# Kernel optimization log

Hardware: AMD Instinct MI355X
Metric: run time of the kernel (lower is better)

The kernel has to match this reference:

```python
import jax, jax.numpy as jnp
import numpy as np

NT, C, B, N, H, E = 32768, 128, 64, 512, 4, 524288  # total nodes, channels, graphs, nodes/graph, heads, edges
DH = C // H
EPS = 1e-5


def batchnorm(x, g, b):
    # BatchNorm1d over the node dimension (training-mode batch statistics)
    m = x.mean(axis=0)
    v = x.var(axis=0)
    return (x - m) * jax.lax.rsqrt(v + EPS) * g + b


def setup_inputs() -> dict:
    key = jax.random.key(0)
    ks = jax.random.split(key, 8)
    s = 1.0 / np.sqrt(C)
    return dict(
        x=jax.random.normal(ks[0], (NT, C), jnp.float32),
        edge_index=jax.random.randint(ks[1], (2, E), 0, NT, dtype=jnp.int32),
        Wc=jax.random.normal(ks[2], (C, C), jnp.float32) * s,
        bc=jnp.zeros((C,), jnp.float32),
        in_proj_w=jax.random.normal(ks[3], (3 * C, C), jnp.float32) * s,
        in_proj_b=jnp.zeros((3 * C,), jnp.float32),
        out_proj_w=jax.random.normal(ks[4], (C, C), jnp.float32) * s,
        out_proj_b=jnp.zeros((C,), jnp.float32),
        gn1=jnp.ones((C,), jnp.float32), bn1=jnp.zeros((C,), jnp.float32),
        gn2=jnp.ones((C,), jnp.float32), bn2=jnp.zeros((C,), jnp.float32),
        gn3=jnp.ones((C,), jnp.float32), bn3=jnp.zeros((C,), jnp.float32),
        Wm1=jax.random.normal(ks[5], (2 * C, C), jnp.float32) * s,
        bm1=jnp.zeros((2 * C,), jnp.float32),
        Wm2=jax.random.normal(ks[6], (C, 2 * C), jnp.float32) / np.sqrt(2 * C),
        bm2=jnp.zeros((C,), jnp.float32),
    )


def reference(x, edge_index, Wc, bc, in_proj_w, in_proj_b, out_proj_w, out_proj_b,
              gn1, bn1, gn2, bn2, gn3, bn3, Wm1, bm1, Wm2, bm2):
    # --- local branch: mean-aggregation message passing + linear + residual + BN ---
    src, dst = edge_index[0], edge_index[1]
    agg = jax.ops.segment_sum(x[src], dst, num_segments=NT)            # [NT, C]
    cnt = jax.ops.segment_sum(jnp.ones((E, 1), x.dtype), dst, num_segments=NT)
    agg = agg / jnp.maximum(cnt, 1.0)
    h_local = agg @ Wc.T + bc + x                                       # dropout p=0 -> no-op
    h_local = batchnorm(h_local, gn1, bn1)

    # --- global branch: to_dense_batch (equal-size graphs -> reshape) + MHA ---
    hd = x.reshape(B, N, C)
    qkv = hd @ in_proj_w.T + in_proj_b                                  # [B, N, 3C]
    q, k, v = jnp.split(qkv, 3, axis=-1)
    q = q.reshape(B, N, H, DH).transpose(0, 2, 1, 3)                    # [B, H, N, DH]
    k = k.reshape(B, N, H, DH).transpose(0, 2, 1, 3)
    v = v.reshape(B, N, H, DH).transpose(0, 2, 1, 3)
    scores = jnp.einsum('bhqd,bhkd->bhqk', q, k) / np.sqrt(DH)          # [B, H, N, N]
    attn = jax.nn.softmax(scores, axis=-1)
    o = jnp.einsum('bhqk,bhkd->bhqd', attn, v)                          # [B, H, N, DH]
    o = o.transpose(0, 2, 1, 3).reshape(B, N, C)
    h_attn = (o @ out_proj_w.T + out_proj_b).reshape(NT, C) + x
    h_attn = batchnorm(h_attn, gn2, bn2)

    # --- combine + MLP + final norm ---
    out = h_local + h_attn
    out = out + (jax.nn.relu(out @ Wm1.T + bm1) @ Wm2.T + bm2)
    return batchnorm(out, gn3, bn3)
```

## Files before the change

kernel.cpp:

```cpp
#include <hip/hip_runtime.h>
#include <cstddef>

#define NT    32768
#define CCH   128
#define BB    64
#define NNODE 512
#define NHEAD 4
#define DHEAD 32
#define EE    524288
#define EPS   1e-5f
#define MAXDEG 96

typedef unsigned short u16;
typedef unsigned int   u32;
typedef __attribute__((ext_vector_type(8))) short short8;
typedef __attribute__((ext_vector_type(4))) short short4v;
typedef __attribute__((ext_vector_type(4))) float f32x4;

__device__ __forceinline__ float b2f(u32 w) { return __uint_as_float(w << 16); }
__device__ __forceinline__ u16 f2b(float f) {
    u32 u = __float_as_uint(f);
    u += 0x7FFF + ((u >> 16) & 1);
    return (u16)(u >> 16);
}

__global__ __launch_bounds__(256) void prep_kernel(const float* __restrict__ x,
                                                   const float* __restrict__ Wc,
                                                   const float* __restrict__ Wqkv,
                                                   const float* __restrict__ Wo,
                                                   const float* __restrict__ Wm1,
                                                   const float* __restrict__ Wm2,
                                                   u16* __restrict__ xb,
                                                   u16* __restrict__ Wcb,
                                                   u16* __restrict__ Wqkvb,
                                                   u16* __restrict__ Wob,
                                                   u16* __restrict__ Wm1b,
                                                   u16* __restrict__ Wm2b,
                                                   const int* __restrict__ ei,
                                                   int* __restrict__ cursor,
                                                   int* __restrict__ bucket) {
    if (blockIdx.x >= 2120) {
        int e = (blockIdx.x - 2120) * 256 + threadIdx.x;
        int src = ei[e];
        int dst = ei[EE + e];
        int pos = atomicAdd(cursor + dst, 1);
        if (pos < MAXDEG) bucket[dst * MAXDEG + pos] = src;
        return;
    }
    int r = blockIdx.x * 256 + threadIdx.x;
    const float* src; u16* dst;
    if (r < 524288) { src = x; dst = xb; }
    else if ((r -= 524288) < 2048) { src = Wc; dst = Wcb; }
    else if ((r -= 2048) < 6144) { src = Wqkv; dst = Wqkvb; }
    else if ((r -= 6144) < 2048) { src = Wo; dst = Wob; }
    else if ((r -= 2048) < 4096) { src = Wm1; dst = Wm1b; }
    else { r -= 4096; src = Wm2; dst = Wm2b; }
    size_t base = (size_t)r * 8;
    float4 a = *(const float4*)(src + base);
    float4 b = *(const float4*)(src + base + 4);
    uint4 u;
    u.x = (u32)f2b(a.x) | ((u32)f2b(a.y) << 16);
    u.y = (u32)f2b(a.z) | ((u32)f2b(a.w) << 16);
    u.z = (u32)f2b(b.x) | ((u32)f2b(b.y) << 16);
    u.w = (u32)f2b(b.z) | ((u32)f2b(b.w) << 16);
    *(uint4*)(dst + base) = u;
}

__global__ __launch_bounds__(256) void aggregate(const int* __restrict__ bucket,
                                                 const int* __restrict__ cursor,
                                                 const u16* __restrict__ xb,
                                                 u16* __restrict__ agg) {
    int ln = threadIdx.x >> 5;
    int c4 = threadIdx.x & 31;
    int n = blockIdx.x * 8 + ln;
    __shared__ int srcs[8][MAXDEG];
    int d = min(cursor[n], MAXDEG);
    for (int j = c4; j < d; j += 32) srcs[ln][j] = bucket[n * MAXDEG + j];
    __syncthreads();
    float s0 = 0.f, s1 = 0.f, s2 = 0.f, s3 = 0.f;
    for (int j = 0; j < d; ++j) {
        uint2 w = *(const uint2*)(xb + (size_t)srcs[ln][j] * CCH + c4 * 4);
        s0 += b2f(w.x & 0xffffu);
        s1 += b2f(w.x >> 16);
        s2 += b2f(w.y & 0xffffu);
        s3 += b2f(w.y >> 16);
    }
    float inv = 1.0f / fmaxf((float)d, 1.0f);
    uint2 out;
    out.x = (u32)f2b(s0 * inv) | ((u32)f2b(s1 * inv) << 16);
    out.y = (u32)f2b(s2 * inv) | ((u32)f2b(s3 * inv) << 16);
    *(uint2*)(agg + (size_t)n * CCH + c4 * 4) = out;
}

template <bool RELU, int RESID, bool STATS>
__global__ __launch_bounds__(256) void gemm_mfma(const u16* __restrict__ A,
                                                 const u16* __restrict__ W,
                                                 const float* __restrict__ bias,
                                                 const u16* __restrict__ residb,
                                                 u16* __restrict__ outb,
                                                 float* __restrict__ sum,
                                                 float* __restrict__ sumsq,
                                                 int M, int N, int K) {
    __shared__ u16 As[128 * 32];
    __shared__ u16 Bs[128 * 32];
    __shared__ float csum[128];
    __shared__ float csq[128];
    int m0 = blockIdx.x * 128, n0 = blockIdx.y * 128;
    int tid = threadIdx.x;
    int lane = tid & 63, wave = tid >> 6;
    int wm = (wave & 1) * 64, wn = (wave >> 1) * 64;
    int l15 = lane & 15, l4 = lane >> 4;

    if (STATS) {
        if (tid < 128) { csum[tid] = 0.f; csq[tid] = 0.f; }
    }

    f32x4 zero = {0.f, 0.f, 0.f, 0.f};
    f32x4 acc[4][4];
#pragma unroll
    for (int i = 0; i < 4; ++i)
#pragma unroll
        for (int j = 0; j < 4; ++j) acc[i][j] = zero;

    int srow = tid >> 2;
    int scol = (tid & 3) * 8;

    for (int k0 = 0; k0 < K; k0 += 32) {
        uint4 a0 = *(const uint4*)(A + (size_t)(m0 + srow) * K + k0 + scol);
        uint4 a1 = *(const uint4*)(A + (size_t)(m0 + srow + 64) * K + k0 + scol);
        uint4 b0 = *(const uint4*)(W + (size_t)(n0 + srow) * K + k0 + scol);
        uint4 b1 = *(const uint4*)(W + (size_t)(n0 + srow + 64) * K + k0 + scol);
        __syncthreads();
        *(uint4*)&As[srow * 32 + scol] = a0;
        *(uint4*)&As[(srow + 64) * 32 + scol] = a1;
        *(uint4*)&Bs[srow * 32 + scol] = b0;
        *(uint4*)&Bs[(srow + 64) * 32 + scol] = b1;
        __syncthreads();
        short8 af[4], bf[4];
#pragma unroll
        for (int t = 0; t < 4; ++t) {
            af[t] = *(const short8*)&As[(wm + t * 16 + l15) * 32 + l4 * 8];
            bf[t] = *(const short8*)&Bs[(wn + t * 16 + l15) * 32 + l4 * 8];
        }
#pragma unroll
        for (int mt = 0; mt < 4; ++mt)
#pragma unroll
            for (int nt = 0; nt < 4; ++nt)
                acc[mt][nt] = __builtin_amdgcn_mfma_f32_16x16x32_bf16(af[mt], bf[nt], acc[mt][nt], 0, 0, 0);
    }

#pragma unroll
    for (int nt = 0; nt < 4; ++nt) {
        int col = n0 + wn + nt * 16 + l15;
        float bs = bias[col];
        float ps = 0.f, pq = 0.f;
#pragma unroll
        for (int mt = 0; mt < 4; ++mt) {
#pragma unroll
            for (int r = 0; r < 4; ++r) {
                int row = m0 + wm + mt * 16 + l4 * 4 + r;
                float v = acc[mt][nt][r] + bs;
                if (RESID == 2) v += b2f(residb[(size_t)row * N + col]);
                if (RELU) v = fmaxf(v, 0.0f);
                outb[(size_t)row * N + col] = f2b(v);
                if (STATS) { ps += v; pq += v * v; }
            }
        }
        if (STATS) {
            atomicAdd(&csum[wn + nt * 16 + l15], ps);
            atomicAdd(&csq[wn + nt * 16 + l15], pq);
        }
    }
    if (STATS) {
        __syncthreads();
        if (tid < 128) {
            atomicAdd(sum + n0 + tid, csum[tid]);
            atomicAdd(sumsq + n0 + tid, csq[tid]);
        }
    }
}

__global__ __launch_bounds__(256) void gemm_wc_qkv(const u16* __restrict__ aggb,
                                                   const u16* __restrict__ Wcb,
                                                   const float* __restrict__ bc,
                                                   const u16* __restrict__ xb,
                                                   u16* __restrict__ hlocb,
                                                   float* __restrict__ sum1,
                                                   float* __restrict__ sq1,
                                                   const u16* __restrict__ Wqkvb,
                                                   const float* __restrict__ bqkv,
                                                   u16* __restrict__ qkvb) {
    __shared__ u16 As[128 * 32];
    __shared__ u16 Bs[128 * 32];
    __shared__ float csum[128];
    __shared__ float csq[128];
    int y = blockIdx.y;
    bool wc = (y == 0);
    const u16* A = wc ? aggb : xb;
    const u16* W = wc ? Wcb : (Wqkvb + (size_t)(y - 1) * 128 * 128);
    const float* bias = wc ? bc : (bqkv + (y - 1) * 128);
    int ostride = wc ? 128 : 384;
    int ocol0 = wc ? 0 : (y - 1) * 128;
    u16* outp = wc ? hlocb : qkvb;

    int m0 = blockIdx.x * 128;
    int tid = threadIdx.x;
    int lane = tid & 63, wave = tid >> 6;
    int wm = (wave & 1) * 64, wn = (wave >> 1) * 64;
    int l15 = lane & 15, l4 = lane >> 4;

    if (wc && tid < 128) { csum[tid] = 0.f; csq[tid] = 0.f; }

    f32x4 zero = {0.f, 0.f, 0.f, 0.f};
    f32x4 acc[4][4];
#pragma unroll
    for (int i = 0; i < 4; ++i)
#pragma unroll
        for (int j = 0; j < 4; ++j) acc[i][j] = zero;

    int srow = tid >> 2;
    int scol = (tid & 3) * 8;

    for (int k0 = 0; k0 < 128; k0 += 32) {
        uint4 a0 = *(const uint4*)(A + (size_t)(m0 + srow) * 128 + k0 + scol);
        uint4 a1 = *(const uint4*)(A + (size_t)(m0 + srow + 64) * 128 + k0 + scol);
        uint4 b0 = *(const uint4*)(W + (size_t)srow * 128 + k0 + scol);
        uint4 b1 = *(const uint4*)(W + (size_t)(srow + 64) * 128 + k0 + scol);
        __syncthreads();
        *(uint4*)&As[srow * 32 + scol] = a0;
        *(uint4*)&As[(srow + 64) * 32 + scol] = a1;
        *(uint4*)&Bs[srow * 32 + scol] = b0;
        *(uint4*)&Bs[(srow + 64) * 32 + scol] = b1;
        __syncthreads();
        short8 af[4], bf[4];
#pragma unroll
        for (int t = 0; t < 4; ++t) {
            af[t] = *(const short8*)&As[(wm + t * 16 + l15) * 32 + l4 * 8];
            bf[t] = *(const short8*)&Bs[(wn + t * 16 + l15) * 32 + l4 * 8];
        }
#pragma unroll
        for (int mt = 0; mt < 4; ++mt)
#pragma unroll
            for (int nt = 0; nt < 4; ++nt)
                acc[mt][nt] = __builtin_amdgcn_mfma_f32_16x16x32_bf16(af[mt], bf[nt], acc[mt][nt], 0, 0, 0);
    }

#pragma unroll
    for (int nt = 0; nt < 4; ++nt) {
        int lcol = wn + nt * 16 + l15;
        float bs = bias[lcol];
        float ps = 0.f, pq = 0.f;
#pragma unroll
        for (int mt = 0; mt < 4; ++mt) {
#pragma unroll
            for (int r = 0; r < 4; ++r) {
                int row = m0 + wm + mt * 16 + l4 * 4 + r;
                float v = acc[mt][nt][r] + bs;
                if (wc) v += b2f(xb[(size_t)row * 128 + lcol]);
                outp[(size_t)row * ostride + ocol0 + lcol] = f2b(v);
                if (wc) { ps += v; pq += v * v; }
            }
        }
        if (wc) {
            atomicAdd(&csum[lcol], ps);
            atomicAdd(&csq[lcol], pq);
        }
    }
    if (wc) {
        __syncthreads();
        if (tid < 128) {
            atomicAdd(sum1 + tid, csum[tid]);
            atomicAdd(sq1 + tid, csq[tid]);
        }
    }
}

__global__ __launch_bounds__(256) void gemm_m1c(const u16* __restrict__ hlocb,
                                                const u16* __restrict__ t2b,
                                                const float* __restrict__ sum1,
                                                const float* __restrict__ sq1,
                                                const float* __restrict__ g1,
                                                const float* __restrict__ bt1,
                                                const float* __restrict__ sum2,
                                                const float* __restrict__ sq2,
                                                const float* __restrict__ g2,
                                                const float* __restrict__ bt2,
                                                u16* __restrict__ shb,
                                                const u16* __restrict__ Wm1b,
                                                const float* __restrict__ bm1,
                                                u16* __restrict__ hidb) {
    __shared__ u16 As[128 * 32];
    __shared__ u16 Bs[128 * 32];
    __shared__ float AF1[128], BF1[128], AF2[128], BF2[128];
    int tid = threadIdx.x;
    {
        int c = tid & 127;
        const float* sm = (tid < 128) ? sum1 : sum2;
        const float* sq = (tid < 128) ? sq1 : sq2;
        const float* g  = (tid < 128) ? g1 : g2;
        const float* bt = (tid < 128) ? bt1 : bt2;
        float m = sm[c] * (1.0f / NT);
        float v = sq[c] * (1.0f / NT) - m * m;
        float a = g[c] * rsqrtf(v + EPS);
        if (tid < 128) { AF1[c] = a; BF1[c] = bt[c] - m * a; }
        else           { AF2[c] = a; BF2[c] = bt[c] - m * a; }
    }
    int m0 = blockIdx.x * 128, n0 = blockIdx.y * 128;
    int lane = tid & 63, wave = tid >> 6;
    int wm = (wave & 1) * 64, wn = (wave >> 1) * 64;
    int l15 = lane & 15, l4 = lane >> 4;

    f32x4 zero = {0.f, 0.f, 0.f, 0.f};
    f32x4 acc[4][4];
#pragma unroll
    for (int i = 0; i < 4; ++i)
#pragma unroll
        for (int j = 0; j < 4; ++j) acc[i][j] = zero;

    int srow = tid >> 2;
    int scol = (tid & 3) * 8;
    bool wr = (blockIdx.y == 0);

    for (int k0 = 0; k0 < 128; k0 += 32) {
        uint4 h0 = *(const uint4*)(hlocb + (size_t)(m0 + srow) * 128 + k0 + scol);
        uint4 h1 = *(const uint4*)(hlocb + (size_t)(m0 + srow + 64) * 128 + k0 + scol);
        uint4 t0 = *(const uint4*)(t2b + (size_t)(m0 + srow) * 128 + k0 + scol);
        uint4 t1 = *(const uint4*)(t2b + (size_t)(m0 + srow + 64) * 128 + k0 + scol);
        uint4 b0 = *(const uint4*)(Wm1b + (size_t)(n0 + srow) * 128 + k0 + scol);
        uint4 b1 = *(const uint4*)(Wm1b + (size_t)(n0 + srow + 64) * 128 + k0 + scol);
        __syncthreads();
        uint4 c0, c1;
        {
            const u32 hw[4] = {h0.x, h0.y, h0.z, h0.w};
            const u32 tw[4] = {t0.x, t0.y, t0.z, t0.w};
            u32 ow[4];
#pragma unroll
            for (int p = 0; p < 4; ++p) {
                int cc = k0 + scol + p * 2;
                float v0 = AF1[cc] * b2f(hw[p] & 0xffffu) + BF1[cc] + AF2[cc] * b2f(tw[p] & 0xffffu) + BF2[cc];
                float v1 = AF1[cc + 1] * b2f(hw[p] >> 16) + BF1[cc + 1] + AF2[cc + 1] * b2f(tw[p] >> 16) + BF2[cc + 1];
                ow[p] = (u32)f2b(v0) | ((u32)f2b(v1) << 16);
            }
            c0.x = ow[0]; c0.y = ow[1]; c0.z = ow[2]; c0.w = ow[3];
        }
        {
            const u32 hw[4] = {h1.x, h1.y, h1.z, h1.w};
            const u32 tw[4] = {t1.x, t1.y, t1.z, t1.w};
            u32 ow[4];
#pragma unroll
            for (int p = 0; p < 4; ++p) {
                int cc = k0 + scol + p * 2;
                float v0 = AF1[cc] * b2f(hw[p] & 0xffffu) + BF1[cc] + AF2[cc] * b2f(tw[p] & 0xffffu) + BF2[cc];
                float v1 = AF1[cc + 1] * b2f(hw[p] >> 16) + BF1[cc + 1] + AF2[cc + 1] * b2f(tw[p] >> 16) + BF2[cc + 1];
                ow[p] = (u32)f2b(v0) | ((u32)f2b(v1) << 16);
            }
            c1.x = ow[0]; c1.y = ow[1]; c1.z = ow[2]; c1.w = ow[3];
        }
        *(uint4*)&As[srow * 32 + scol] = c0;
        *(uint4*)&As[(srow + 64) * 32 + scol] = c1;
        *(uint4*)&Bs[srow * 32 + scol] = b0;
        *(uint4*)&Bs[(srow + 64) * 32 + scol] = b1;
        if (wr) {
            *(uint4*)(shb + (size_t)(m0 + srow) * 128 + k0 + scol) = c0;
            *(uint4*)(shb + (size_t)(m0 + srow + 64) * 128 + k0 + scol) = c1;
        }
        __syncthreads();
        short8 af[4], bf[4];
#pragma unroll
        for (int t = 0; t < 4; ++t) {
            af[t] = *(const short8*)&As[(wm + t * 16 + l15) * 32 + l4 * 8];
            bf[t] = *(const short8*)&Bs[(wn + t * 16 + l15) * 32 + l4 * 8];
        }
#pragma unroll
        for (int mt = 0; mt < 4; ++mt)
#pragma unroll
            for (int nt = 0; nt < 4; ++nt)
                acc[mt][nt] = __builtin_amdgcn_mfma_f32_16x16x32_bf16(af[mt], bf[nt], acc[mt][nt], 0, 0, 0);
    }

#pragma unroll
    for (int nt = 0; nt < 4; ++nt) {
        int col = n0 + wn + nt * 16 + l15;
        float bs = bm1[col];
#pragma unroll
        for (int mt = 0; mt < 4; ++mt) {
#pragma unroll
            for (int r = 0; r < 4; ++r) {
                int row = m0 + wm + mt * 16 + l4 * 4 + r;
                float v = fmaxf(acc[mt][nt][r] + bs, 0.0f);
                hidb[(size_t)row * 256 + col] = f2b(v);
            }
        }
    }
}

__global__ __launch_bounds__(256) void final_bn(const u16* __restrict__ X,
                                                const float* __restrict__ sum3,
                                                const float* __restrict__ sq3,
                                                const float* __restrict__ g3,
                                                const float* __restrict__ bt3,
                                                float* __restrict__ outp) {
    __shared__ float A3[128], B3[128];
    int t = threadIdx.x;
    if (t < 128) {
        float m = sum3[t] * (1.0f / NT);
        float v = sq3[t] * (1.0f / NT) - m * m;
        float a = g3[t] * rsqrtf(v + EPS);
        A3[t] = a;
        B3[t] = bt3[t] - m * a;
    }
    __syncthreads();
    int i8 = blockIdx.x * 256 + t;
    size_t i = (size_t)i8 * 8;
    int c = (int)(i & (CCH - 1));
    uint4 u = *(const uint4*)(X + i);
    float x[8];
    x[0] = b2f(u.x & 0xffffu); x[1] = b2f(u.x >> 16);
    x[2] = b2f(u.y & 0xffffu); x[3] = b2f(u.y >> 16);
    x[4] = b2f(u.z & 0xffffu); x[5] = b2f(u.z >> 16);
    x[6] = b2f(u.w & 0xffffu); x[7] = b2f(u.w >> 16);
    float4 o0, o1;
    o0.x = A3[c + 0] * x[0] + B3[c + 0];
    o0.y = A3[c + 1] * x[1] + B3[c + 1];
    o0.z = A3[c + 2] * x[2] + B3[c + 2];
    o0.w = A3[c + 3] * x[3] + B3[c + 3];
    o1.x = A3[c + 4] * x[4] + B3[c + 4];
    o1.y = A3[c + 5] * x[5] + B3[c + 5];
    o1.z = A3[c + 6] * x[6] + B3[c + 6];
    o1.w = A3[c + 7] * x[7] + B3[c + 7];
    *(float4*)(outp + i) = o0;
    *(float4*)(outp + i + 4) = o1;
}

__global__ __launch_bounds__(512) void attn_mfma(const u16* __restrict__ qkv,
                                                 u16* __restrict__ o) {
    __shared__ __align__(16) u16 Ks[512 * 40];
    __shared__ __align__(16) u16 Vt[32 * 520];
    int bh = blockIdx.x;
    int b = bh >> 2, h = bh & 3;
    int tid = threadIdx.x;
    int lane = tid & 63, wave = tid >> 6;
    int quad = lane >> 4, l15 = lane & 15;
    const float scale = 0.1767766952966369f;

    const u16* kvbase = qkv + (size_t)b * 512 * 384 + 128 + h * 32;
    for (int idx = tid; idx < 2048; idx += 512) {
        int row = idx >> 2, c = idx & 3;
        *(uint4*)&Ks[row * 40 + c * 8] = *(const uint4*)(kvbase + (size_t)row * 384 + c * 8);
    }
    for (int idx = tid; idx < 2048; idx += 512) {
        int row = idx >> 2, c = idx & 3;
        uint4 u = *(const uint4*)(kvbase + 128 + (size_t)row * 384 + c * 8);
        u16 e[8];
        *(uint4*)e = u;
#pragma unroll
        for (int i = 0; i < 8; ++i) Vt[(c * 8 + i) * 520 + row] = e[i];
    }
    __syncthreads();

    f32x4 zero = {0.f, 0.f, 0.f, 0.f};
    for (int qt = 0; qt < 4; ++qt) {
        int qbase = wave * 64 + qt * 16;
        short8 qf = *(const short8*)(qkv + (size_t)(b * 512 + qbase + l15) * 384 + h * 32 + quad * 8);
        float lq = 0.f;
        f32x4 oa[2] = {zero, zero};

        for (int kv0 = 0; kv0 < 512; kv0 += 64) {
            f32x4 s[4];
#pragma unroll
            for (int t = 0; t < 4; ++t) {
                short8 kb = *(const short8*)&Ks[(kv0 + t * 16 + l15) * 40 + quad * 8];
                s[t] = __builtin_amdgcn_mfma_f32_16x16x32_bf16(kb, qf, zero, 0, 0, 0);
            }
            short8 pa[4];
#pragma unroll
            for (int t = 0; t < 4; ++t) {
                float p0 = __expf(s[t][0] * scale);
                float p1 = __expf(s[t][1] * scale);
                float p2 = __expf(s[t][2] * scale);
                float p3 = __expf(s[t][3] * scale);
                lq += (p0 + p1) + (p2 + p3);
                short8 a8 = {(short)f2b(p0), (short)f2b(p1), (short)f2b(p2), (short)f2b(p3), 0, 0, 0, 0};
                pa[t] = a8;
            }
#pragma unroll
            for (int t = 0; t < 4; ++t) {
                int tbase = kv0 + t * 16;
#pragma unroll
                for (int n = 0; n < 2; ++n) {
                    short4v v4 = *(const short4v*)&Vt[(n * 16 + l15) * 520 + tbase + quad * 4];
                    short8 vb = {v4.x, v4.y, v4.z, v4.w, 0, 0, 0, 0};
                    oa[n] = __builtin_amdgcn_mfma_f32_16x16x32_bf16(pa[t], vb, oa[n], 0, 0, 0);
                }
            }
        }
        lq += __shfl_xor(lq, 16);
        lq += __shfl_xor(lq, 32);
        u16* op = o + (size_t)(b * 512 + qbase) * 128 + h * 32;
#pragma unroll
        for (int r = 0; r < 4; ++r) {
            float Lr = __shfl(lq, quad * 4 + r);
            float inv = 1.0f / Lr;
#pragma unroll
            for (int n = 0; n < 2; ++n)
                op[(quad * 4 + r) * 128 + n * 16 + l15] = f2b(oa[n][r] * inv);
        }
    }
}

extern "C" void kernel_launch(void* const* d_in, const int* in_sizes, int n_in,
                              void* d_out, int out_size, void* d_ws, size_t ws_size,
                              hipStream_t stream) {
    const float* x    = (const float*)d_in[0];
    const int*   ei   = (const int*)d_in[1];
    const float* Wc   = (const float*)d_in[2];
    const float* bc   = (const float*)d_in[3];
    const float* Wqkv = (const float*)d_in[4];
    const float* bqkv = (const float*)d_in[5];
    const float* Wo   = (const float*)d_in[6];
    const float* bo   = (const float*)d_in[7];
    const float* gn1  = (const float*)d_in[8];
    const float* bn1b = (const float*)d_in[9];
    const float* gn2  = (const float*)d_in[10];
    const float* bn2b = (const float*)d_in[11];
    const float* gn3  = (const float*)d_in[12];
    const float* bn3b = (const float*)d_in[13];
    const float* Wm1  = (const float*)d_in[14];
    const float* bm1  = (const float*)d_in[15];
    const float* Wm2  = (const float*)d_in[16];
    const float* bm2  = (const float*)d_in[17];
    float* outp = (float*)d_out;

    char* w = (char*)d_ws;
    const size_t MB = 1024 * 1024;
    u16* xb    = (u16*)(w);
    u16* hlocb = (u16*)(w + 8 * MB);
    u16* t2b   = (u16*)(w + 16 * MB);
    u16* out2b = (u16*)(w + 24 * MB);
    u16* qkvb  = (u16*)(w + 32 * MB);
    u16* hidb  = (u16*)(w + 56 * MB);
    u16* shb   = (u16*)(w + 72 * MB);
    int* bucket = (int*)(w + 80 * MB);
    int* cursor = (int*)(w + 92 * MB);
    float* stats = (float*)(w + 92 * MB + 128 * 1024);
    u16* Wcb   = (u16*)(w + 93 * MB);
    u16* Wqkvb = Wcb + 16384;
    u16* Wob   = Wqkvb + 49152;
    u16* Wm1b  = Wob + 16384;
    u16* Wm2b  = Wm1b + 32768;
    float* sum1 = stats;        float* sq1 = stats + 128;
    float* sum2 = stats + 256;  float* sq2 = stats + 384;
    float* sum3 = stats + 512;  float* sq3 = stats + 640;

    hipMemsetAsync(cursor, 0, 128 * 1024 + 6 * 128 * 4, stream);

    prep_kernel<<<2120 + 2048, 256, 0, stream>>>(x, Wc, Wqkv, Wo, Wm1, Wm2,
                                                 xb, Wcb, Wqkvb, Wob, Wm1b, Wm2b,
                                                 ei, cursor, bucket);

    aggregate<<<NT / 8, 256, 0, stream>>>(bucket, cursor, xb, shb);

    {
        dim3 g(NT / 128, 4);
        gemm_wc_qkv<<<g, 256, 0, stream>>>(shb, Wcb, bc, xb, hlocb, sum1, sq1,
                                           Wqkvb, bqkv, qkvb);
    }

    attn_mfma<<<BB * NHEAD, 512, 0, stream>>>(qkvb, shb);

    {
        dim3 g(NT / 128, 1);
        gemm_mfma<false, 2, true><<<g, 256, 0, stream>>>(
            shb, Wob, bo, xb, t2b, sum2, sq2, NT, 128, 128);
    }

    {
        dim3 g(NT / 128, 2);
        gemm_m1c<<<g, 256, 0, stream>>>(hlocb, t2b, sum1, sq1, gn1, bn1b,
                                        sum2, sq2, gn2, bn2b, shb, Wm1b, bm1, hidb);
    }

    {
        dim3 g(NT / 128, 1);
        gemm_mfma<false, 2, true><<<g, 256, 0, stream>>>(
            hidb, Wm2b, bm2, shb, out2b, sum3, sq3, NT, 128, 256);
    }

    final_bn<<<NT * CCH / 8 / 256, 256, 0, stream>>>(out2b, sum3, sq3, gn3, bn3b, outp);
}
```

Measured before the change: 254.6 us.

## Prefetch next K-tile into registers and stage GEMM epilogue through LDS

In the three bf16 MFMA GEMM kernels, the global loads for the next K slice are now issued while the current slice sits in LDS. This software pipeline hides load latency behind the MFMA loop. The epilogue now writes each 16x64 output tile into a per-wave padded LDS buffer and stores it with 16-byte row-contiguous writes, replacing the 2-byte scattered stores. The cost is extra LDS, which may lower occupancy, plus more live registers for the prefetched tiles.

```diff
diff --git a/kernel.cpp b/kernel.cpp
--- a/kernel.cpp
+++ b/kernel.cpp
@@ -103,6 +103,7 @@
                                                  int M, int N, int K) {
     __shared__ u16 As[128 * 32];
     __shared__ u16 Bs[128 * 32];
+    __shared__ u16 Cs[4][16 * 72];
     __shared__ float csum[128];
     __shared__ float csq[128];
     int m0 = blockIdx.x * 128, n0 = blockIdx.y * 128;
@@ -125,16 +126,24 @@
     int srow = tid >> 2;
     int scol = (tid & 3) * 8;
 
-    for (int k0 = 0; k0 < K; k0 += 32) {
-        uint4 a0 = *(const uint4*)(A + (size_t)(m0 + srow) * K + k0 + scol);
-        uint4 a1 = *(const uint4*)(A + (size_t)(m0 + srow + 64) * K + k0 + scol);
-        uint4 b0 = *(const uint4*)(W + (size_t)(n0 + srow) * K + k0 + scol);
-        uint4 b1 = *(const uint4*)(W + (size_t)(n0 + srow + 64) * K + k0 + scol);
-        __syncthreads();
+    int kIter = K >> 5;
+    uint4 a0 = *(const uint4*)(A + (size_t)(m0 + srow) * K + scol);
+    uint4 a1 = *(const uint4*)(A + (size_t)(m0 + srow + 64) * K + scol);
+    uint4 b0 = *(const uint4*)(W + (size_t)(n0 + srow) * K + scol);
+    uint4 b1 = *(const uint4*)(W + (size_t)(n0 + srow + 64) * K + scol);
+    for (int ki = 0; ki < kIter; ++ki) {
+        if (ki) __syncthreads();
         *(uint4*)&As[srow * 32 + scol] = a0;
         *(uint4*)&As[(srow + 64) * 32 + scol] = a1;
         *(uint4*)&Bs[srow * 32 + scol] = b0;
         *(uint4*)&Bs[(srow + 64) * 32 + scol] = b1;
+        if (ki + 1 < kIter) {
+            int k0 = (ki + 1) * 32;
+            a0 = *(const uint4*)(A + (size_t)(m0 + srow) * K + k0 + scol);
+            a1 = *(const uint4*)(A + (size_t)(m0 + srow + 64) * K + k0 + scol);
+            b0 = *(const uint4*)(W + (size_t)(n0 + srow) * K + k0 + scol);
+            b1 = *(const uint4*)(W + (size_t)(n0 + srow + 64) * K + k0 + scol);
+        }
         __syncthreads();
         short8 af[4], bf[4];
 #pragma unroll
@@ -149,29 +158,40 @@
                 acc[mt][nt] = __builtin_amdgcn_mfma_f32_16x16x32_bf16(af[mt], bf[nt], acc[mt][nt], 0, 0, 0);
     }
 
-#pragma unroll
-    for (int nt = 0; nt < 4; ++nt) {
-        int col = n0 + wn + nt * 16 + l15;
-        float bs = bias[col];
-        float ps = 0.f, pq = 0.f;
-#pragma unroll
-        for (int mt = 0; mt < 4; ++mt) {
+    float ps[4] = {0.f, 0.f, 0.f, 0.f};
+    float pq[4] = {0.f, 0.f, 0.f, 0.f};
+    int rl = lane >> 3;
+    int cg = lane & 7;
+#pragma unroll
+    for (int mt = 0; mt < 4; ++mt) {
+#pragma unroll
+        for (int nt = 0; nt < 4; ++nt) {
+            int col = n0 + wn + nt * 16 + l15;
+            float bs = bias[col];
 #pragma unroll
             for (int r = 0; r < 4; ++r) {
                 int row = m0 + wm + mt * 16 + l4 * 4 + r;
                 float v = acc[mt][nt][r] + bs;
                 if (RESID == 2) v += b2f(residb[(size_t)row * N + col]);
                 if (RELU) v = fmaxf(v, 0.0f);
-                outb[(size_t)row * N + col] = f2b(v);
-                if (STATS) { ps += v; pq += v * v; }
-            }
-        }
-        if (STATS) {
-            atomicAdd(&csum[wn + nt * 16 + l15], ps);
-            atomicAdd(&csq[wn + nt * 16 + l15], pq);
+                Cs[wave][(l4 * 4 + r) * 72 + nt * 16 + l15] = f2b(v);
+                if (STATS) { ps[nt] += v; pq[nt] += v * v; }
+            }
+        }
+#pragma unroll
+        for (int p = 0; p < 2; ++p) {
+            int lrow = p * 8 + rl;
+            uint4 wv = *(const uint4*)&Cs[wave][lrow * 72 + cg * 8];
+            int grow = m0 + wm + mt * 16 + lrow;
+            *(uint4*)(outb + (size_t)grow * N + n0 + wn + cg * 8) = wv;
         }
     }
     if (STATS) {
+#pragma unroll
+        for (int nt = 0; nt < 4; ++nt) {
+            atomicAdd(&csum[wn + nt * 16 + l15], ps[nt]);
+            atomicAdd(&csq[wn + nt * 16 + l15], pq[nt]);
+        }
         __syncthreads();
         if (tid < 128) {
             atomicAdd(sum + n0 + tid, csum[tid]);
@@ -192,6 +212,7 @@
                                                    u16* __restrict__ qkvb) {
     __shared__ u16 As[128 * 32];
     __shared__ u16 Bs[128 * 32];
+    __shared__ u16 Cs[4][16 * 72];
     __shared__ float csum[128];
     __shared__ float csq[128];
     int y = blockIdx.y;
@@ -221,16 +242,23 @@
     int srow = tid >> 2;
     int scol = (tid & 3) * 8;
 
-    for (int k0 = 0; k0 < 128; k0 += 32) {
-        uint4 a0 = *(const uint4*)(A + (size_t)(m0 + srow) * 128 + k0 + scol);
-        uint4 a1 = *(const uint4*)(A + (size_t)(m0 + srow + 64) * 128 + k0 + scol);
-        uint4 b0 = *(const uint4*)(W + (size_t)srow * 128 + k0 + scol);
-        uint4 b1 = *(const uint4*)(W + (size_t)(srow + 64) * 128 + k0 + scol);
-        __syncthreads();
+    uint4 a0 = *(const uint4*)(A + (size_t)(m0 + srow) * 128 + scol);
+    uint4 a1 = *(const uint4*)(A + (size_t)(m0 + srow + 64) * 128 + scol);
+    uint4 b0 = *(const uint4*)(W + (size_t)srow * 128 + scol);
+    uint4 b1 = *(const uint4*)(W + (size_t)(srow + 64) * 128 + scol);
+    for (int ki = 0; ki < 4; ++ki) {
+        if (ki) __syncthreads();
         *(uint4*)&As[srow * 32 + scol] = a0;
         *(uint4*)&As[(srow + 64) * 32 + scol] = a1;
         *(uint4*)&Bs[srow * 32 + scol] = b0;
         *(uint4*)&Bs[(srow + 64) * 32 + scol] = b1;
+        if (ki < 3) {
+            int k0 = (ki + 1) * 32;
+            a0 = *(const uint4*)(A + (size_t)(m0 + srow) * 128 + k0 + scol);
+            a1 = *(const uint4*)(A + (size_t)(m0 + srow + 64) * 128 + k0 + scol);
+            b0 = *(const uint4*)(W + (size_t)srow * 128 + k0 + scol);
+            b1 = *(const uint4*)(W + (size_t)(srow + 64) * 128 + k0 + scol);
+        }
         __syncthreads();
         short8 af[4], bf[4];
 #pragma unroll
@@ -245,28 +273,39 @@
                 acc[mt][nt] = __builtin_amdgcn_mfma_f32_16x16x32_bf16(af[mt], bf[nt], acc[mt][nt], 0, 0, 0);
     }
 
-#pragma unroll
-    for (int nt = 0; nt < 4; ++nt) {
-        int lcol = wn + nt * 16 + l15;
-        float bs = bias[lcol];
-        float ps = 0.f, pq = 0.f;
-#pragma unroll
-        for (int mt = 0; mt < 4; ++mt) {
+    float ps[4] = {0.f, 0.f, 0.f, 0.f};
+    float pq[4] = {0.f, 0.f, 0.f, 0.f};
+    int rl = lane >> 3;
+    int cg = lane & 7;
+#pragma unroll
+    for (int mt = 0; mt < 4; ++mt) {
+#pragma unroll
+        for (int nt = 0; nt < 4; ++nt) {
+            int lcol = wn + nt * 16 + l15;
+            float bs = bias[lcol];
 #pragma unroll
             for (int r = 0; r < 4; ++r) {
                 int row = m0 + wm + mt * 16 + l4 * 4 + r;
                 float v = acc[mt][nt][r] + bs;
                 if (wc) v += b2f(xb[(size_t)row * 128 + lcol]);
-                outp[(size_t)row * ostride + ocol0 + lcol] = f2b(v);
-                if (wc) { ps += v; pq += v * v; }
-            }
-        }
-        if (wc) {
-            atomicAdd(&csum[lcol], ps);
-            atomicAdd(&csq[lcol], pq);
+                Cs[wave][(l4 * 4 + r) * 72 + nt * 16 + l15] = f2b(v);
+                if (wc) { ps[nt] += v; pq[nt] += v * v; }
+            }
+        }
+#pragma unroll
+        for (int p = 0; p < 2; ++p) {
+            int lrow = p * 8 + rl;
+            uint4 wv = *(const uint4*)&Cs[wave][lrow * 72 + cg * 8];
+            int grow = m0 + wm + mt * 16 + lrow;
+            *(uint4*)(outp + (size_t)grow * ostride + ocol0 + wn + cg * 8) = wv;
         }
     }
     if (wc) {
+#pragma unroll
+        for (int nt = 0; nt < 4; ++nt) {
+            atomicAdd(&csum[wn + nt * 16 + l15], ps[nt]);
+            atomicAdd(&csq[wn + nt * 16 + l15], pq[nt]);
+        }
         __syncthreads();
         if (tid < 128) {
             atomicAdd(sum1 + tid, csum[tid]);
@@ -291,6 +330,7 @@
                                                 u16* __restrict__ hidb) {
     __shared__ u16 As[128 * 32];
     __shared__ u16 Bs[128 * 32];
+    __shared__ u16 Cs[4][16 * 72];
     __shared__ float AF1[128], BF1[128], AF2[128], BF2[128];
     int tid = threadIdx.x;
     {
@@ -321,14 +361,16 @@
     int scol = (tid & 3) * 8;
     bool wr = (blockIdx.y == 0);
 
-    for (int k0 = 0; k0 < 128; k0 += 32) {
-        uint4 h0 = *(const uint4*)(hlocb + (size_t)(m0 + srow) * 128 + k0 + scol);
-        uint4 h1 = *(const uint4*)(hlocb + (size_t)(m0 + srow + 64) * 128 + k0 + scol);
-        uint4 t0 = *(const uint4*)(t2b + (size_t)(m0 + srow) * 128 + k0 + scol);
-        uint4 t1 = *(const uint4*)(t2b + (size_t)(m0 + srow + 64) * 128 + k0 + scol);
-        uint4 b0 = *(const uint4*)(Wm1b + (size_t)(n0 + srow) * 128 + k0 + scol);
-        uint4 b1 = *(const uint4*)(Wm1b + (size_t)(n0 + srow + 64) * 128 + k0 + scol);
-        __syncthreads();
+    uint4 h0 = *(const uint4*)(hlocb + (size_t)(m0 + srow) * 128 + scol);
+    uint4 h1 = *(const uint4*)(hlocb + (size_t)(m0 + srow + 64) * 128 + scol);
+    uint4 t0 = *(const uint4*)(t2b + (size_t)(m0 + srow) * 128 + scol);
+    uint4 t1 = *(const uint4*)(t2b + (size_t)(m0 + srow + 64) * 128 + scol);
+    uint4 b0 = *(const uint4*)(Wm1b + (size_t)(n0 + srow) * 128 + scol);
+    uint4 b1 = *(const uint4*)(Wm1b + (size_t)(n0 + srow + 64) * 128 + scol);
+    __syncthreads();
+    for (int ki = 0; ki < 4; ++ki) {
+        int k0 = ki * 32;
+        if (ki) __syncthreads();
         uint4 c0, c1;
         {
             const u32 hw[4] = {h0.x, h0.y, h0.z, h0.w};
@@ -364,6 +406,15 @@
             *(uint4*)(shb + (size_t)(m0 + srow) * 128 + k0 + scol) = c0;
             *(uint4*)(shb + (size_t)(m0 + srow + 64) * 128 + k0 + scol) = c1;
         }
+        if (ki < 3) {
+            int kn = k0 + 32;
+            h0 = *(const uint4*)(hlocb + (size_t)(m0 + srow) * 128 + kn + scol);
+            h1 = *(const uint4*)(hlocb + (size_t)(m0 + srow + 64) * 128 + kn + scol);
+            t0 = *(const uint4*)(t2b + (size_t)(m0 + srow) * 128 + kn + scol);
+            t1 = *(const uint4*)(t2b + (size_t)(m0 + srow + 64) * 128 + kn + scol);
+            b0 = *(const uint4*)(Wm1b + (size_t)(n0 + srow) * 128 + kn + scol);
+            b1 = *(const uint4*)(Wm1b + (size_t)(n0 + srow + 64) * 128 + kn + scol);
+        }
         __syncthreads();
         short8 af[4], bf[4];
 #pragma unroll
@@ -378,18 +429,26 @@
                 acc[mt][nt] = __builtin_amdgcn_mfma_f32_16x16x32_bf16(af[mt], bf[nt], acc[mt][nt], 0, 0, 0);
     }
 
-#pragma unroll
-    for (int nt = 0; nt < 4; ++nt) {
-        int col = n0 + wn + nt * 16 + l15;
-        float bs = bm1[col];
-#pragma unroll
-        for (int mt = 0; mt < 4; ++mt) {
+    int rl = lane >> 3;
+    int cg = lane & 7;
+#pragma unroll
+    for (int mt = 0; mt < 4; ++mt) {
+#pragma unroll
+        for (int nt = 0; nt < 4; ++nt) {
+            int col = n0 + wn + nt * 16 + l15;
+            float bs = bm1[col];
 #pragma unroll
             for (int r = 0; r < 4; ++r) {
-                int row = m0 + wm + mt * 16 + l4 * 4 + r;
                 float v = fmaxf(acc[mt][nt][r] + bs, 0.0f);
-                hidb[(size_t)row * 256 + col] = f2b(v);
-            }
+                Cs[wave][(l4 * 4 + r) * 72 + nt * 16 + l15] = f2b(v);
+            }
+        }
+#pragma unroll
+        for (int p = 0; p < 2; ++p) {
+            int lrow = p * 8 + rl;
+            uint4 wv = *(const uint4*)&Cs[wave][lrow * 72 + cg * 8];
+            int grow = m0 + wm + mt * 16 + lrow;
+            *(uint4*)(hidb + (size_t)grow * 256 + n0 + wn + cg * 8) = wv;
         }
     }
 }
```

Result: faster. 249.0 us (-2.2%).
